# Kernel optimization log

Measured on AMD Instinct MI355X. Metric: run time of the kernel, lower is better.

Reference implementation:

```python
import jax, jax.numpy as jnp
import numpy as np

N_HEAD = 16
LORA_RANK = 16
ROPE_BASE = 10000.0


def _rope_cos_sin(T, D, dtype):
    # GPT-NeoX style rotate-half RoPE tables, shape [T, D]
    inv_freq = 1.0 / (ROPE_BASE ** (jnp.arange(0, D, 2, dtype=jnp.float32) / D))
    t = jnp.arange(T, dtype=jnp.float32)
    freqs = t[:, None] * inv_freq[None, :]          # [T, D/2]
    emb = jnp.concatenate([freqs, freqs], axis=-1)   # [T, D]
    return jnp.cos(emb).astype(dtype), jnp.sin(emb).astype(dtype)


def _rotate_half(x):
    x1, x2 = jnp.split(x, 2, axis=-1)
    return jnp.concatenate([-x2, x1], axis=-1)


def _apply_rope(q, k, cos, sin):
    # q,k: [B,H,T,D]; cos,sin: [T,D]
    c = cos[None, None, :, :]
    s = sin[None, None, :, :]
    return q * c + _rotate_half(q) * s, k * c + _rotate_half(k) * s


def setup_inputs() -> dict:
    key = jax.random.key(0)
    ks = jax.random.split(key, 6)
    B, T, C = 4, 1024, 2048
    r = LORA_RANK
    sc = 1.0 / np.sqrt(C)
    return {
        "x": jax.random.normal(ks[0], (B, T, C), jnp.float32),
        "qkvo_delta": jax.random.normal(ks[1], (B, 8 * r, C), jnp.float32) * 0.02,
        "Wq": jax.random.normal(ks[2], (C, C), jnp.float32) * sc,
        "Wk": jax.random.normal(ks[3], (C, C), jnp.float32) * sc,
        "Wv": jax.random.normal(ks[4], (C, C), jnp.float32) * sc,
        "Wo": jax.random.normal(ks[5], (C, C), jnp.float32) * sc,
    }


def reference(x, qkvo_delta, Wq, Wk, Wv, Wo):
    B, T, C = x.shape
    H = N_HEAD
    D = C // H

    # split LoRA deltas: each [B, r, C]
    dqA, dqB, dkA, dkB, dvA, dvB, doA, doB = jnp.split(qkvo_delta, 8, axis=1)

    def merged(W, dB, dA):
        # W [out,in] + dB^T @ dA -> [B, out, in]
        return W[None] + jnp.einsum('bro,bri->boi', dB, dA)

    def proj(inp, Wm):
        # inp @ Wm^T (per-batch merged weight)
        return jnp.einsum('bti,boi->bto', inp, Wm)

    q = proj(x, merged(Wq, dqB, dqA))
    k = proj(x, merged(Wk, dkB, dkA))
    v = proj(x, merged(Wv, dvB, dvA))

    # [B,T,C] -> [B,H,T,D]
    def heads(t):
        return t.reshape(B, T, H, D).transpose(0, 2, 1, 3)

    q, k, v = heads(q), heads(k), heads(v)

    cos, sin = _rope_cos_sin(T, D, x.dtype)
    q, k = _apply_rope(q, k, cos, sin)

    # full (non-causal) SDPA, matching is_causal=False in the source
    scale = 1.0 / np.sqrt(D)
    scores = jnp.einsum('bhtd,bhsd->bhts', q, k) * scale
    attn = jax.nn.softmax(scores, axis=-1)
    y = jnp.einsum('bhts,bhsd->bhtd', attn, v)

    y = y.transpose(0, 2, 1, 3).reshape(B, T, C)
    out = proj(y, merged(Wo, doB, doA))
    return out
```

## Files before the change

### kernel.cpp

```cpp
#include <hip/hip_runtime.h>
#include <cstdint>
#include <cstddef>

typedef __attribute__((ext_vector_type(8))) __bf16 bf8_t;
typedef __attribute__((ext_vector_type(8))) short s8_t;
typedef __attribute__((ext_vector_type(4))) short s4_t;
typedef __attribute__((ext_vector_type(4))) float f4_t;

__device__ __forceinline__ float bf2f(unsigned short h) {
  union { unsigned u; float f; } v; v.u = (unsigned)h << 16; return v.f;
}
__device__ __forceinline__ unsigned short f2bf(float f) {
  union { float f; unsigned u; } v; v.f = f;
  return (unsigned short)((v.u + 0x7FFFu + ((v.u >> 16) & 1u)) >> 16);
}

#define GL16(gp, lp) __builtin_amdgcn_global_load_lds( \
    (__attribute__((address_space(1))) void*)(gp),     \
    (__attribute__((address_space(3))) void*)(lp), 16, 0, 0)

__global__ void k_f32_to_bf16(const float* __restrict__ in,
                              unsigned short* __restrict__ out, int n4) {
  int i = blockIdx.x * blockDim.x + threadIdx.x;
  if (i >= n4) return;
  float4 v = reinterpret_cast<const float4*>(in)[i];
  s4_t o;
  o.x = (short)f2bf(v.x); o.y = (short)f2bf(v.y);
  o.z = (short)f2bf(v.z); o.w = (short)f2bf(v.w);
  reinterpret_cast<s4_t*>(out)[i] = o;
}

__global__ void k_rope_table(float* __restrict__ cosT, float* __restrict__ sinT) {
  int t = blockIdx.x, d = threadIdx.x;
  float inv = exp2f(-(float)d * (13.287712379549449f / 64.0f));
  float ang = (float)t * inv;
  cosT[t * 64 + d] = cosf(ang);
  sinT[t * 64 + d] = sinf(ang);
}

__global__ __launch_bounds__(256) void k_lora_mfma(
    const unsigned short* __restrict__ X,
    const unsigned short* __restrict__ dlb,
    float* __restrict__ u, int pstart, int pcount) {
  __shared__ __align__(16) unsigned short Xs[64 * 64];
  __shared__ __align__(16) unsigned short Da[64 * 64];
  const int t = threadIdx.x;
  const int b = blockIdx.y;
  const int m0 = blockIdx.x * 64;
  const int w = t >> 6, lane = t & 63, lr = lane & 15, lg = lane >> 4;
  const int nrow = pcount * 16;
  f4_t acc[4] = {};
  for (int k0 = 0; k0 < 2048; k0 += 64) {
    __syncthreads();
#pragma unroll
    for (int i = 0; i < 2; ++i) {
      int idx = i * 256 + t;
      int row = idx >> 3, c = idx & 7;
      GL16(X + ((size_t)b * 1024 + m0 + row) * 2048 + k0 + ((c ^ (row & 7)) * 8),
           Xs + (size_t)idx * 8);
      int ric = row < nrow ? row : nrow - 1;
      int g = (pstart + (ric >> 4)) * 32 + (ric & 15);
      GL16(dlb + ((size_t)b * 128 + g) * 2048 + k0 + ((c ^ (ric & 7)) * 8),
           Da + (size_t)idx * 8);
    }
    __syncthreads();
#pragma unroll
    for (int kk = 0; kk < 2; ++kk) {
      bf8_t af = *(const bf8_t*)&Xs[(w * 16 + lr) * 64 + (((kk * 4 + lg) ^ (lr & 7)) * 8)];
#pragma unroll
      for (int n = 0; n < 4; ++n) {
        if (n < pcount) {
          bf8_t bfv = *(const bf8_t*)&Da[(n * 16 + lr) * 64 + (((kk * 4 + lg) ^ (lr & 7)) * 8)];
          acc[n] = __builtin_amdgcn_mfma_f32_16x16x32_bf16(af, bfv, acc[n], 0, 0, 0);
        }
      }
    }
  }
#pragma unroll
  for (int n = 0; n < 4; ++n) {
    if (n < pcount) {
#pragma unroll
      for (int j = 0; j < 4; ++j)
        u[(((size_t)b * 4 + pstart + n) * 16 + lr) * 1024 + m0 + w * 16 + lg * 4 + j] = acc[n][j];
    }
  }
}

struct GArgs {
  const unsigned short *Bw0, *Bw1, *Bw2;
  void *o0, *o1, *o2;
  int m0_, m1_, m2_;
  int p0_, p1_, p2_;
};
#define BM 128
#define BN 128
#define BKK 64
__global__ __launch_bounds__(256, 2) void k_gemm(
    const unsigned short* __restrict__ A,
    GArgs ga,
    const float* __restrict__ u,
    const float* __restrict__ dl) {
  constexpr int K = 2048;
  const int z = blockIdx.z;
  const unsigned short* Bw = z == 0 ? ga.Bw0 : (z == 1 ? ga.Bw1 : ga.Bw2);
  void* outv = z == 0 ? ga.o0 : (z == 1 ? ga.o1 : ga.o2);
  const int mode = z == 0 ? ga.m0_ : (z == 1 ? ga.m1_ : ga.m2_);
  const int p = z == 0 ? ga.p0_ : (z == 1 ? ga.p1_ : ga.p2_);
  __shared__ unsigned short As[BM * BKK];
  __shared__ unsigned short Bs[BN * BKK];
  const int t = threadIdx.x;
  const int m0 = blockIdx.y * BM;
  const int n0 = blockIdx.x * BN;
  const int lane = t & 63;
  const int w = t >> 6;
  const int wr = (w >> 1) * 64, wc = (w & 1) * 64;
  const int lr = lane & 15;
  const int lg = lane >> 4;
  const int lk = lg * 8;
  const int srow = t >> 3;
  const int scol = (t & 7) * 8;
  f4_t acc[4][4] = {};

  for (int k0 = 0; k0 < K; k0 += BKK) {
#pragma unroll
    for (int j = 0; j < 4; ++j) {
      int row = j * 32 + srow;
      GL16(A  + (size_t)(m0 + row) * K + k0 + scol, As + row * BKK + scol);
      GL16(Bw + (size_t)(n0 + row) * K + k0 + scol, Bs + row * BKK + scol);
    }
    __syncthreads();
#pragma unroll
    for (int kk = 0; kk < BKK; kk += 32) {
      bf8_t af[4], bfr[4];
#pragma unroll
      for (int m = 0; m < 4; ++m)
        af[m] = *(const bf8_t*)&As[(wr + m * 16 + lr) * BKK + kk + lk];
#pragma unroll
      for (int n = 0; n < 4; ++n)
        bfr[n] = *(const bf8_t*)&Bs[(wc + n * 16 + lr) * BKK + kk + lk];
#pragma unroll
      for (int m = 0; m < 4; ++m)
#pragma unroll
        for (int n = 0; n < 4; ++n)
          acc[m][n] = __builtin_amdgcn_mfma_f32_16x16x32_bf16(af[m], bfr[n], acc[m][n], 0, 0, 0);
    }
    __syncthreads();
  }

  const int b = m0 >> 10;
  const int t0r = m0 & 1023;
  for (int idx = t; idx < 128 * 32; idx += 256) {
    int rr = idx >> 5, r = idx & 31;
    float val = (r < 16) ? u[(((size_t)b * 4 + p) * 16 + r) * 1024 + t0r + rr] : 0.0f;
    As[rr * 32 + r] = f2bf(val);
  }
  for (int idx = t; idx < 128 * 32; idx += 256) {
    int cc = idx >> 5, r = idx & 31;
    float val = (r < 16) ? dl[((size_t)b * 128 + p * 32 + 16 + r) * 2048 + n0 + cc] : 0.0f;
    Bs[cc * 32 + r] = f2bf(val);
  }
  __syncthreads();
  {
    bf8_t af[4], bfr[4];
#pragma unroll
    for (int m = 0; m < 4; ++m)
      af[m] = *(const bf8_t*)&As[(wr + m * 16 + lr) * 32 + lk];
#pragma unroll
    for (int n = 0; n < 4; ++n)
      bfr[n] = *(const bf8_t*)&Bs[(wc + n * 16 + lr) * 32 + lk];
#pragma unroll
    for (int m = 0; m < 4; ++m)
#pragma unroll
      for (int n = 0; n < 4; ++n)
        acc[m][n] = __builtin_amdgcn_mfma_f32_16x16x32_bf16(af[m], bfr[n], acc[m][n], 0, 0, 0);
  }

  unsigned short* out16 = (unsigned short*)outv;
  float* out32 = (float*)outv;
#pragma unroll
  for (int m = 0; m < 4; ++m) {
    int ri = wr + m * 16 + lg * 4;
#pragma unroll
    for (int j = 0; j < 4; ++j) {
      int grow = m0 + ri + j;
      int gb = grow >> 10, gt = grow & 1023;
#pragma unroll
      for (int n = 0; n < 4; ++n) {
        int gcol = n0 + wc + n * 16 + lr;
        float fv = acc[m][n][j];
        if (mode == 0) {
          size_t dst = (((size_t)gb * 16 + (gcol >> 7)) * 1024 + gt) * 128 + (gcol & 127);
          out16[dst] = f2bf(fv);
        } else if (mode == 1) {
          size_t dst = (((size_t)gb * 16 + (gcol >> 7)) * 128 + (gcol & 127)) * 1024 + gt;
          out16[dst] = f2bf(fv);
        } else {
          out32[(size_t)grow * 2048 + gcol] = fv;
        }
      }
    }
  }
}

__global__ void k_rope(unsigned short* __restrict__ X,
                       const float* __restrict__ cosT, const float* __restrict__ sinT) {
  int idx = blockIdx.x * 256 + threadIdx.x;
  int d0 = (idx & 7) * 8;
  int tt = (idx >> 3) & 1023;
  size_t base = (size_t)(idx >> 3) * 128 + d0;
  s8_t a = *(s8_t*)&X[base];
  s8_t bb = *(s8_t*)&X[base + 64];
  float4 c0 = *(const float4*)&cosT[tt * 64 + d0];
  float4 c1 = *(const float4*)&cosT[tt * 64 + d0 + 4];
  float4 sv0 = *(const float4*)&sinT[tt * 64 + d0];
  float4 sv1 = *(const float4*)&sinT[tt * 64 + d0 + 4];
  float cv[8] = {c0.x, c0.y, c0.z, c0.w, c1.x, c1.y, c1.z, c1.w};
  float sw[8] = {sv0.x, sv0.y, sv0.z, sv0.w, sv1.x, sv1.y, sv1.z, sv1.w};
  s8_t ra, rb;
#pragma unroll
  for (int j = 0; j < 8; ++j) {
    float av = bf2f((unsigned short)a[j]);
    float bv = bf2f((unsigned short)bb[j]);
    ra[j] = (short)f2bf(av * cv[j] - bv * sw[j]);
    rb[j] = (short)f2bf(bv * cv[j] + av * sw[j]);
  }
  *(s8_t*)&X[base] = ra;
  *(s8_t*)&X[base + 64] = rb;
}

__global__ __launch_bounds__(512, 4) void k_attn(
    const unsigned short* __restrict__ Qg,
    const unsigned short* __restrict__ Kg,
    const unsigned short* __restrict__ Vt,
    unsigned short* __restrict__ Y) {
  const float scale = 0.08838834764831845f;
  const float L2E = 1.4426950408889634f;
  const int bid = blockIdx.x;
  const int wg = (bid & 7) * 64 + (bid >> 3);
  const int bh = wg >> 3;
  const int b = bh >> 4, h = bh & 15;
  const int t = threadIdx.x;
  const int w = t >> 6, lane = t & 63;
  const int lr = lane & 15, lg = lane >> 4;
  const int q0 = (wg & 7) * 128 + w * 16;
  const unsigned short* Q  = Qg + (size_t)bh * 131072;
  const unsigned short* Kp = Kg + (size_t)bh * 131072;
  const unsigned short* Vp = Vt + (size_t)bh * 131072;
  __shared__ __align__(16) unsigned short Ks[64 * 128];
  __shared__ __align__(16) unsigned short Vs[128 * 64];
  __shared__ __align__(16) unsigned short Ps[8][16 * 80];
  unsigned short* Pw = Ps[w];

  bf8_t qf[4];
#pragma unroll
  for (int kk = 0; kk < 4; ++kk)
    qf[kk] = *(const bf8_t*)&Q[(size_t)(q0 + lr) * 128 + kk * 32 + lg * 8];

  f4_t o[8] = {};
  float m_run = -1e30f, l_run = 0.0f;

  for (int s0 = 0; s0 < 1024; s0 += 64) {
    __syncthreads();
#pragma unroll
    for (int i = 0; i < 2; ++i) {
      int idx = i * 512 + t;
      int s = idx >> 4, c = t & 15;
      GL16(Kp + (size_t)(s0 + s) * 128 + ((c ^ (s & 7)) * 8), Ks + (size_t)idx * 8);
    }
#pragma unroll
    for (int i = 0; i < 2; ++i) {
      int idx = i * 512 + t;
      int d = idx >> 3, c = t & 7;
      GL16(Vp + (size_t)d * 1024 + s0 + ((c ^ (d & 7)) * 8), Vs + (size_t)idx * 8);
    }
    __syncthreads();

    f4_t sf[4];
#pragma unroll
    for (int ss = 0; ss < 4; ++ss) {
      f4_t c = {0.0f, 0.0f, 0.0f, 0.0f};
#pragma unroll
      for (int kk = 0; kk < 4; ++kk) {
        bf8_t kf = *(const bf8_t*)&Ks[(ss * 16 + lr) * 128 + (((kk * 4 + lg) ^ (lr & 7)) * 8)];
        c = __builtin_amdgcn_mfma_f32_16x16x32_bf16(kf, qf[kk], c, 0, 0, 0);
      }
      sf[ss] = c;
    }
    float vmax = -1e30f;
#pragma unroll
    for (int ss = 0; ss < 4; ++ss)
#pragma unroll
      for (int j = 0; j < 4; ++j) vmax = fmaxf(vmax, sf[ss][j]);
    vmax = fmaxf(vmax, __shfl_xor(vmax, 16));
    vmax = fmaxf(vmax, __shfl_xor(vmax, 32));
    float m_new = fmaxf(m_run, vmax * scale);
    float ratio = exp2f((m_run - m_new) * L2E);
    float lsum = 0.0f;
    float ps[4][4];
#pragma unroll
    for (int ss = 0; ss < 4; ++ss)
#pragma unroll
      for (int j = 0; j < 4; ++j) {
        float pv = exp2f((sf[ss][j] * scale - m_new) * L2E);
        ps[ss][j] = pv; lsum += pv;
      }
    lsum += __shfl_xor(lsum, 16);
    lsum += __shfl_xor(lsum, 32);
    l_run = l_run * ratio + lsum;
    m_run = m_new;
    float rq[4];
#pragma unroll
    for (int j = 0; j < 4; ++j) rq[j] = __shfl(ratio, lg * 4 + j);
#pragma unroll
    for (int n = 0; n < 8; ++n)
#pragma unroll
      for (int j = 0; j < 4; ++j) o[n][j] *= rq[j];
#pragma unroll
    for (int ss = 0; ss < 4; ++ss) {
      s4_t pk;
      pk.x = (short)f2bf(ps[ss][0]); pk.y = (short)f2bf(ps[ss][1]);
      pk.z = (short)f2bf(ps[ss][2]); pk.w = (short)f2bf(ps[ss][3]);
      *(s4_t*)&Pw[lr * 80 + ss * 16 + lg * 4] = pk;
    }
    bf8_t pa0 = *(const bf8_t*)&Pw[lr * 80 + lg * 8];
    bf8_t pa1 = *(const bf8_t*)&Pw[lr * 80 + 32 + lg * 8];
#pragma unroll
    for (int n = 0; n < 8; ++n) {
      int d = n * 16 + lr;
      bf8_t v0 = *(const bf8_t*)&Vs[d * 64 + (((0 + lg) ^ (lr & 7)) * 8)];
      bf8_t v1 = *(const bf8_t*)&Vs[d * 64 + (((4 + lg) ^ (lr & 7)) * 8)];
      o[n] = __builtin_amdgcn_mfma_f32_16x16x32_bf16(pa0, v0, o[n], 0, 0, 0);
      o[n] = __builtin_amdgcn_mfma_f32_16x16x32_bf16(pa1, v1, o[n], 0, 0, 0);
    }
  }

  float linv[4];
#pragma unroll
  for (int j = 0; j < 4; ++j) linv[j] = 1.0f / __shfl(l_run, lg * 4 + j);
#pragma unroll
  for (int n = 0; n < 8; ++n)
#pragma unroll
    for (int j = 0; j < 4; ++j) {
      int qg = q0 + lg * 4 + j;
      Y[((size_t)b * 1024 + qg) * 2048 + h * 128 + n * 16 + lr] =
          f2bf(o[n][j] * linv[j]);
    }
}

extern "C" void kernel_launch(void* const* d_in, const int* in_sizes, int n_in,
                              void* d_out, int out_size, void* d_ws, size_t ws_size,
                              hipStream_t stream) {
  const float* x  = (const float*)d_in[0];
  const float* dl = (const float*)d_in[1];
  const float* W[4] = {(const float*)d_in[2], (const float*)d_in[3],
                       (const float*)d_in[4], (const float*)d_in[5]};
  char* ws = (char*)d_ws;
  size_t off = 0;
  auto take = [&](size_t bytes) {
    void* p = ws + off; off += (bytes + 255) & ~(size_t)255; return p;
  };
  unsigned short* xb = (unsigned short*)take(8388608ull * 2);
  unsigned short* Wb[4];
  for (int i = 0; i < 4; ++i) Wb[i] = (unsigned short*)take(4194304ull * 2);
  unsigned short* qb = (unsigned short*)take(8388608ull * 2);
  unsigned short* kb = (unsigned short*)take(8388608ull * 2);
  unsigned short* vT = (unsigned short*)take(8388608ull * 2);
  unsigned short* y  = (unsigned short*)take(8388608ull * 2);
  float* u    = (float*)take(4ull * 4 * 16 * 1024 * 4);
  float* cosT = (float*)take(1024ull * 64 * 4);
  float* sinT = (float*)take(1024ull * 64 * 4);
  unsigned short* dlb = (unsigned short*)take(1048576ull * 2);
  if (off > ws_size) return;

  k_f32_to_bf16<<<8192, 256, 0, stream>>>(x, xb, 2097152);
  for (int i = 0; i < 4; ++i)
    k_f32_to_bf16<<<4096, 256, 0, stream>>>(W[i], Wb[i], 1048576);
  k_f32_to_bf16<<<1024, 256, 0, stream>>>(dl, dlb, 262144);
  k_rope_table<<<1024, 64, 0, stream>>>(cosT, sinT);
  k_lora_mfma<<<dim3(16, 4), 256, 0, stream>>>(xb, dlb, u, 0, 3);

  GArgs gq;
  gq.Bw0 = Wb[0]; gq.o0 = qb;    gq.m0_ = 0; gq.p0_ = 0;
  gq.Bw1 = Wb[1]; gq.o1 = kb;    gq.m1_ = 0; gq.p1_ = 1;
  gq.Bw2 = Wb[2]; gq.o2 = vT;    gq.m2_ = 1; gq.p2_ = 2;
  k_gemm<<<dim3(16, 32, 3), 256, 0, stream>>>(xb, gq, u, dl);

  k_rope<<<2048, 256, 0, stream>>>(qb, cosT, sinT);
  k_rope<<<2048, 256, 0, stream>>>(kb, cosT, sinT);
  k_attn<<<512, 512, 0, stream>>>(qb, kb, vT, y);
  k_lora_mfma<<<dim3(16, 4), 256, 0, stream>>>(y, dlb, u, 3, 1);

  GArgs go;
  go.Bw0 = Wb[3]; go.o0 = d_out; go.m0_ = 2; go.p0_ = 3;
  go.Bw1 = Wb[3]; go.o1 = d_out; go.m1_ = 2; go.p1_ = 3;
  go.Bw2 = Wb[3]; go.o2 = d_out; go.m2_ = 2; go.p2_ = 3;
  k_gemm<<<dim3(16, 32, 1), 256, 0, stream>>>(y, go, u, dl);
}
```

Before: 380.8 us.

## Replace GEMM with 256x256 double-buffered, swizzled, software-pipelined kernel

Replaces the 128x128 single-buffered projection GEMM with a 256x256-tile, 512-thread kernel. It double-buffers LDS with fine-grained vmcnt waits and raw barriers, applies an XOR swizzle to LDS rows, raises MFMA priority, and remaps block IDs for L2 locality. Q/K/V are fused along N in one 1D grid. The goal is to overlap global loads with MFMA work and raise arithmetic intensity. The cost is 128KB of LDS, heavier register pressure, and only 384/128 workgroups, which may underfill the GPU for the output projection.

```diff
diff --git a/kernel.cpp b/kernel.cpp
--- a/kernel.cpp
+++ b/kernel.cpp
@@ -18,6 +18,11 @@
 #define GL16(gp, lp) __builtin_amdgcn_global_load_lds( \
     (__attribute__((address_space(1))) void*)(gp),     \
     (__attribute__((address_space(3))) void*)(lp), 16, 0, 0)
+
+#define WAITV(N) do { asm volatile("s_waitcnt vmcnt(" #N ")" ::: "memory"); \
+                      __builtin_amdgcn_sched_barrier(0); } while (0)
+#define BAR() do { __builtin_amdgcn_s_barrier(); \
+                   __builtin_amdgcn_sched_barrier(0); } while (0)
 
 __global__ void k_f32_to_bf16(const float* __restrict__ in,
                               unsigned short* __restrict__ out, int n4) {
@@ -86,120 +91,179 @@
   }
 }
 
-struct GArgs {
-  const unsigned short *Bw0, *Bw1, *Bw2;
+struct G8 {
+  const unsigned short *W0, *W1, *W2;
   void *o0, *o1, *o2;
-  int m0_, m1_, m2_;
-  int p0_, p1_, p2_;
+  int n_nt, fused;
 };
-#define BM 128
-#define BN 128
-#define BKK 64
-__global__ __launch_bounds__(256, 2) void k_gemm(
-    const unsigned short* __restrict__ A,
-    GArgs ga,
-    const float* __restrict__ u,
-    const float* __restrict__ dl) {
-  constexpr int K = 2048;
-  const int z = blockIdx.z;
-  const unsigned short* Bw = z == 0 ? ga.Bw0 : (z == 1 ? ga.Bw1 : ga.Bw2);
-  void* outv = z == 0 ? ga.o0 : (z == 1 ? ga.o1 : ga.o2);
-  const int mode = z == 0 ? ga.m0_ : (z == 1 ? ga.m1_ : ga.m2_);
-  const int p = z == 0 ? ga.p0_ : (z == 1 ? ga.p1_ : ga.p2_);
-  __shared__ unsigned short As[BM * BKK];
-  __shared__ unsigned short Bs[BN * BKK];
+
+__global__ __launch_bounds__(512, 2) void k_gemm8(
+    const unsigned short* __restrict__ Ag, G8 ga,
+    const float* __restrict__ u, const float* __restrict__ dl) {
+  __shared__ unsigned short Ab[2][256 * 64];
+  __shared__ unsigned short Bb[2][256 * 64];
   const int t = threadIdx.x;
-  const int m0 = blockIdx.y * BM;
-  const int n0 = blockIdx.x * BN;
-  const int lane = t & 63;
-  const int w = t >> 6;
-  const int wr = (w >> 1) * 64, wc = (w & 1) * 64;
-  const int lr = lane & 15;
-  const int lg = lane >> 4;
-  const int lk = lg * 8;
-  const int srow = t >> 3;
-  const int scol = (t & 7) * 8;
-  f4_t acc[4][4] = {};
-
-  for (int k0 = 0; k0 < K; k0 += BKK) {
-#pragma unroll
-    for (int j = 0; j < 4; ++j) {
-      int row = j * 32 + srow;
-      GL16(A  + (size_t)(m0 + row) * K + k0 + scol, As + row * BKK + scol);
-      GL16(Bw + (size_t)(n0 + row) * K + k0 + scol, Bs + row * BKK + scol);
-    }
-    __syncthreads();
-#pragma unroll
-    for (int kk = 0; kk < BKK; kk += 32) {
-      bf8_t af[4], bfr[4];
-#pragma unroll
-      for (int m = 0; m < 4; ++m)
-        af[m] = *(const bf8_t*)&As[(wr + m * 16 + lr) * BKK + kk + lk];
-#pragma unroll
-      for (int n = 0; n < 4; ++n)
-        bfr[n] = *(const bf8_t*)&Bs[(wc + n * 16 + lr) * BKK + kk + lk];
-#pragma unroll
-      for (int m = 0; m < 4; ++m)
-#pragma unroll
-        for (int n = 0; n < 4; ++n)
-          acc[m][n] = __builtin_amdgcn_mfma_f32_16x16x32_bf16(af[m], bfr[n], acc[m][n], 0, 0, 0);
-    }
-    __syncthreads();
-  }
+  const int w = t >> 6, l = t & 63;
+  const int lr = l & 15, lg = l >> 4;
+  const int wm = w >> 2, wn = w & 3;
+
+  const int nwg = 16 * ga.n_nt;
+  const int wg = ((int)blockIdx.x & 7) * (nwg >> 3) + ((int)blockIdx.x >> 3);
+  const int m0 = (wg / ga.n_nt) * 256;
+  const int n0 = (wg % ga.n_nt) * 256;
+  const int z = n0 >> 11;
+  const unsigned short* Bg;
+  void* ov;
+  int mode, p, n0i;
+  if (ga.fused) {
+    Bg = z == 0 ? ga.W0 : (z == 1 ? ga.W1 : ga.W2);
+    ov = z == 0 ? ga.o0 : (z == 1 ? ga.o1 : ga.o2);
+    mode = (z == 2) ? 1 : 0; p = z; n0i = n0 & 2047;
+  } else {
+    Bg = ga.W0; ov = ga.o0; mode = 2; p = 3; n0i = n0;
+  }
+
+  f4_t acc[8][4] = {};
+
+#define STAGE_A(tt, par, c) do { \
+  const int k0_ = (tt) * 64; \
+  _Pragma("unroll") for (int rr = 0; rr < 2; ++rr) { \
+    int row_ = (par) * 64 + rr * 128 + w * 8 + (l >> 3); \
+    int col_ = ((l & 7) * 8) ^ ((row_ & 4) ? 16 : 0); \
+    GL16(Ag + (size_t)(m0 + row_) * 2048 + k0_ + col_, \
+         &Ab[c][row_ * 64 + (l & 7) * 8]); \
+  } } while (0)
+
+#define STAGE_B(tt, par, c) do { \
+  const int k0_ = (tt) * 64; \
+  _Pragma("unroll") for (int rr = 0; rr < 2; ++rr) { \
+    int row_ = (par) * 32 + (w & 3) * 8 + (w >> 2) * 64 + rr * 128 + (l >> 3); \
+    int col_ = ((l & 7) * 8) ^ ((row_ & 4) ? 16 : 0); \
+    GL16(Bg + (size_t)(n0i + row_) * 2048 + k0_ + col_, \
+         &Bb[c][row_ * 64 + (l & 7) * 8]); \
+  } } while (0)
+
+#define QUAD(c, mh, nh) do { \
+  const int kc_ = (lr & 4) ? 16 : 0; \
+  bf8_t af_[4][2], bf_[2][2]; \
+  _Pragma("unroll") for (int i = 0; i < 4; ++i) { \
+    int row_ = wm * 128 + (mh) * 64 + i * 16 + lr; \
+    af_[i][0] = *(const bf8_t*)&Ab[c][row_ * 64 + ((lg * 8) ^ kc_)]; \
+    af_[i][1] = *(const bf8_t*)&Ab[c][row_ * 64 + 32 + ((lg * 8) ^ kc_)]; \
+  } \
+  _Pragma("unroll") for (int j = 0; j < 2; ++j) { \
+    int row_ = wn * 64 + (nh) * 32 + j * 16 + lr; \
+    bf_[j][0] = *(const bf8_t*)&Bb[c][row_ * 64 + ((lg * 8) ^ kc_)]; \
+    bf_[j][1] = *(const bf8_t*)&Bb[c][row_ * 64 + 32 + ((lg * 8) ^ kc_)]; \
+  } \
+  __builtin_amdgcn_s_setprio(1); \
+  _Pragma("unroll") for (int kk = 0; kk < 2; ++kk) \
+  _Pragma("unroll") for (int i = 0; i < 4; ++i) \
+  _Pragma("unroll") for (int j = 0; j < 2; ++j) \
+    acc[(mh)*4+i][(nh)*2+j] = __builtin_amdgcn_mfma_f32_16x16x32_bf16( \
+        af_[i][kk], bf_[j][kk], acc[(mh)*4+i][(nh)*2+j], 0, 0, 0); \
+  __builtin_amdgcn_s_setprio(0); \
+} while (0)
+
+  STAGE_B(0, 0, 0); STAGE_A(0, 0, 0); STAGE_B(0, 1, 0); STAGE_A(0, 1, 0);
+  STAGE_B(1, 0, 1); STAGE_A(1, 0, 1);
+  WAITV(8); BAR();
+
+#pragma unroll 1
+  for (int tt = 0; tt < 30; tt += 2) {
+    STAGE_B(tt + 1, 1, 1); QUAD(0, 0, 0); WAITV(6); BAR();
+    STAGE_A(tt + 1, 1, 1); QUAD(0, 1, 0); BAR();
+    STAGE_B(tt + 2, 0, 0); QUAD(0, 0, 1); BAR();
+    STAGE_A(tt + 2, 0, 0); QUAD(0, 1, 1); WAITV(8); BAR();
+    STAGE_B(tt + 2, 1, 0); QUAD(1, 0, 0); WAITV(6); BAR();
+    STAGE_A(tt + 2, 1, 0); QUAD(1, 1, 0); BAR();
+    STAGE_B(tt + 3, 0, 1); QUAD(1, 0, 1); BAR();
+    STAGE_A(tt + 3, 0, 1); QUAD(1, 1, 1); WAITV(8); BAR();
+  }
+  STAGE_B(31, 1, 1); QUAD(0, 0, 0); WAITV(6); BAR();
+  STAGE_A(31, 1, 1); QUAD(0, 1, 0); BAR();
+  QUAD(0, 0, 1); BAR();
+  QUAD(0, 1, 1); WAITV(4); BAR();
+  QUAD(1, 0, 0); WAITV(0); BAR();
+  QUAD(1, 1, 0); BAR();
+  QUAD(1, 0, 1); BAR();
+  QUAD(1, 1, 1); BAR();
 
   const int b = m0 >> 10;
   const int t0r = m0 & 1023;
-  for (int idx = t; idx < 128 * 32; idx += 256) {
-    int rr = idx >> 5, r = idx & 31;
-    float val = (r < 16) ? u[(((size_t)b * 4 + p) * 16 + r) * 1024 + t0r + rr] : 0.0f;
-    As[rr * 32 + r] = f2bf(val);
-  }
-  for (int idx = t; idx < 128 * 32; idx += 256) {
-    int cc = idx >> 5, r = idx & 31;
-    float val = (r < 16) ? dl[((size_t)b * 128 + p * 32 + 16 + r) * 2048 + n0 + cc] : 0.0f;
-    Bs[cc * 32 + r] = f2bf(val);
+  {
+    int row = t >> 1, cb = (t & 1) * 16;
+    s8_t v0, v1;
+#pragma unroll
+    for (int r = 0; r < 8; ++r) {
+      int cc = cb + r;
+      v0[r] = (short)((cc < 16) ? f2bf(u[(((size_t)b * 4 + p) * 16 + cc) * 1024 + t0r + row]) : 0);
+    }
+#pragma unroll
+    for (int r = 0; r < 8; ++r) {
+      int cc = cb + 8 + r;
+      v1[r] = (short)((cc < 16) ? f2bf(u[(((size_t)b * 4 + p) * 16 + cc) * 1024 + t0r + row]) : 0);
+    }
+    *(s8_t*)&Ab[0][row * 32 + cb] = v0;
+    *(s8_t*)&Ab[0][row * 32 + cb + 8] = v1;
+    s8_t w0, w1;
+#pragma unroll
+    for (int r = 0; r < 8; ++r) {
+      int cc = cb + r;
+      w0[r] = (short)((cc < 16) ? f2bf(dl[((size_t)b * 128 + p * 32 + 16 + cc) * 2048 + n0i + row]) : 0);
+    }
+#pragma unroll
+    for (int r = 0; r < 8; ++r) {
+      int cc = cb + 8 + r;
+      w1[r] = (short)((cc < 16) ? f2bf(dl[((size_t)b * 128 + p * 32 + 16 + cc) * 2048 + n0i + row]) : 0);
+    }
+    *(s8_t*)&Bb[0][row * 32 + cb] = w0;
+    *(s8_t*)&Bb[0][row * 32 + cb + 8] = w1;
   }
   __syncthreads();
   {
-    bf8_t af[4], bfr[4];
-#pragma unroll
-    for (int m = 0; m < 4; ++m)
-      af[m] = *(const bf8_t*)&As[(wr + m * 16 + lr) * 32 + lk];
-#pragma unroll
-    for (int n = 0; n < 4; ++n)
-      bfr[n] = *(const bf8_t*)&Bs[(wc + n * 16 + lr) * 32 + lk];
-#pragma unroll
-    for (int m = 0; m < 4; ++m)
-#pragma unroll
-      for (int n = 0; n < 4; ++n)
-        acc[m][n] = __builtin_amdgcn_mfma_f32_16x16x32_bf16(af[m], bfr[n], acc[m][n], 0, 0, 0);
-  }
-
-  unsigned short* out16 = (unsigned short*)outv;
-  float* out32 = (float*)outv;
-#pragma unroll
-  for (int m = 0; m < 4; ++m) {
-    int ri = wr + m * 16 + lg * 4;
+    bf8_t afl[8], bfl[4];
+#pragma unroll
+    for (int i = 0; i < 8; ++i)
+      afl[i] = *(const bf8_t*)&Ab[0][(wm * 128 + i * 16 + lr) * 32 + lg * 8];
+#pragma unroll
+    for (int j = 0; j < 4; ++j)
+      bfl[j] = *(const bf8_t*)&Bb[0][(wn * 64 + j * 16 + lr) * 32 + lg * 8];
+#pragma unroll
+    for (int i = 0; i < 8; ++i)
+#pragma unroll
+      for (int j = 0; j < 4; ++j)
+        acc[i][j] = __builtin_amdgcn_mfma_f32_16x16x32_bf16(afl[i], bfl[j], acc[i][j], 0, 0, 0);
+  }
+
+  unsigned short* out16 = (unsigned short*)ov;
+  float* out32 = (float*)ov;
+#pragma unroll
+  for (int i = 0; i < 8; ++i) {
+    int ri = wm * 128 + i * 16 + lg * 4;
 #pragma unroll
     for (int j = 0; j < 4; ++j) {
       int grow = m0 + ri + j;
       int gb = grow >> 10, gt = grow & 1023;
 #pragma unroll
       for (int n = 0; n < 4; ++n) {
-        int gcol = n0 + wc + n * 16 + lr;
-        float fv = acc[m][n][j];
+        int gc = n0i + wn * 64 + n * 16 + lr;
+        float fv = acc[i][n][j];
         if (mode == 0) {
-          size_t dst = (((size_t)gb * 16 + (gcol >> 7)) * 1024 + gt) * 128 + (gcol & 127);
+          size_t dst = (((size_t)gb * 16 + (gc >> 7)) * 1024 + gt) * 128 + (gc & 127);
           out16[dst] = f2bf(fv);
         } else if (mode == 1) {
-          size_t dst = (((size_t)gb * 16 + (gcol >> 7)) * 128 + (gcol & 127)) * 1024 + gt;
+          size_t dst = (((size_t)gb * 16 + (gc >> 7)) * 128 + (gc & 127)) * 1024 + gt;
           out16[dst] = f2bf(fv);
         } else {
-          out32[(size_t)grow * 2048 + gcol] = fv;
+          out32[(size_t)grow * 2048 + gc] = fv;
         }
       }
     }
   }
+#undef STAGE_A
+#undef STAGE_B
+#undef QUAD
 }
 
 __global__ void k_rope(unsigned short* __restrict__ X,
@@ -379,20 +443,20 @@
   k_rope_table<<<1024, 64, 0, stream>>>(cosT, sinT);
   k_lora_mfma<<<dim3(16, 4), 256, 0, stream>>>(xb, dlb, u, 0, 3);
 
-  GArgs gq;
-  gq.Bw0 = Wb[0]; gq.o0 = qb;    gq.m0_ = 0; gq.p0_ = 0;
-  gq.Bw1 = Wb[1]; gq.o1 = kb;    gq.m1_ = 0; gq.p1_ = 1;
-  gq.Bw2 = Wb[2]; gq.o2 = vT;    gq.m2_ = 1; gq.p2_ = 2;
-  k_gemm<<<dim3(16, 32, 3), 256, 0, stream>>>(xb, gq, u, dl);
+  G8 gq;
+  gq.W0 = Wb[0]; gq.W1 = Wb[1]; gq.W2 = Wb[2];
+  gq.o0 = qb;    gq.o1 = kb;    gq.o2 = vT;
+  gq.n_nt = 24;  gq.fused = 1;
+  k_gemm8<<<384, 512, 0, stream>>>(xb, gq, u, dl);
 
   k_rope<<<2048, 256, 0, stream>>>(qb, cosT, sinT);
   k_rope<<<2048, 256, 0, stream>>>(kb, cosT, sinT);
   k_attn<<<512, 512, 0, stream>>>(qb, kb, vT, y);
   k_lora_mfma<<<dim3(16, 4), 256, 0, stream>>>(y, dlb, u, 3, 1);
 
-  GArgs go;
-  go.Bw0 = Wb[3]; go.o0 = d_out; go.m0_ = 2; go.p0_ = 3;
-  go.Bw1 = Wb[3]; go.o1 = d_out; go.m1_ = 2; go.p1_ = 3;
-  go.Bw2 = Wb[3]; go.o2 = d_out; go.m2_ = 2; go.p2_ = 3;
-  k_gemm<<<dim3(16, 32, 1), 256, 0, stream>>>(y, go, u, dl);
-}
+  G8 go;
+  go.W0 = Wb[3]; go.W1 = Wb[3]; go.W2 = Wb[3];
+  go.o0 = d_out; go.o1 = d_out; go.o2 = d_out;
+  go.n_nt = 8;   go.fused = 0;
+  k_gemm8<<<128, 512, 0, stream>>>(y, go, u, dl);
+}
```

After: 526.9 us. +38.4%, slower.
